# Kernel optimization log

Measured on AMD Instinct MI355X. Metric: run time of the kernel, lower is better.

Reference implementation:

```python
import jax, jax.numpy as jnp
import numpy as np

B, N, D, R, K, H, ORD = 2, 64, 256, 128, 16, 256, 3


def _ln(x, g, b, eps=1e-5):
    m = jnp.mean(x, -1, keepdims=True)
    v = jnp.mean((x - m) ** 2, -1, keepdims=True)
    return (x - m) * jax.lax.rsqrt(v + eps) * g + b


def _legendre(x, order):
    # Legendre polynomials P0..P_order via Bonnet recurrence, stacked on last dim
    p = [jnp.ones_like(x), x]
    for n in range(2, order + 1):
        p.append(((2 * n - 1) * x * p[-1] - (n - 1) * p[-2]) / n)
    return jnp.stack(p[: order + 1], axis=-1)


def _mlp(x, w1, b1, w2, b2):
    return jax.nn.silu(x @ w1 + b1) @ w2 + b2


def setup_inputs() -> dict:
    key = jax.random.key(0)
    ks = iter(jax.random.split(key, 40))

    def nrm(shape, s=0.02):
        return jax.random.normal(next(ks), shape, jnp.float32) * s

    node_s = jax.random.normal(next(ks), (B, N, D), jnp.float32)
    dist = jax.random.uniform(next(ks), (B, N, N), jnp.float32, 0.5, 6.0)
    dist = (dist + jnp.swapaxes(dist, 1, 2)) / 2.0  # symmetric distances
    rbf = jax.random.normal(next(ks), (B, N, N, R), jnp.float32)
    rh = jax.random.normal(next(ks), (B, N, N, 3), jnp.float32)
    r_hat = rh / jnp.clip(jnp.linalg.norm(rh, axis=-1, keepdims=True), 1e-6)
    access_mask = jnp.ones((B, N, N), dtype=bool)
    return dict(
        node_s=node_s, dist=dist, rbf=rbf, r_hat=r_hat, access_mask=access_mask,
        ep_w1=nrm((2 * D + R, H)), ep_b1=jnp.zeros(H), ep_w2=nrm((H, D)), ep_b2=jnp.zeros(D),
        tp_w1=nrm((ORD + 1 + R, H)), tp_b1=jnp.zeros(H), tp_w2=nrm((H, D)), tp_b2=jnp.zeros(D),
        ts_w1=nrm((2 * D, H)), ts_b1=jnp.zeros(H), ts_w2=nrm((H, 1)), ts_b2=jnp.zeros(1),
        mix_ln_g=jnp.ones(2 * D), mix_ln_b=jnp.zeros(2 * D),
        mix_w1=nrm((2 * D, H)), mix_b1=jnp.zeros(H), mix_w2=nrm((H, D)), mix_b2=jnp.zeros(D),
        gate_w=nrm((D, D)), gate_b=jnp.zeros(D),
        node_ln_g=jnp.ones(D), node_ln_b=jnp.zeros(D), node_w=nrm((D, D)), node_b=jnp.zeros(D),
        edge_ln_g=jnp.ones(D), edge_ln_b=jnp.zeros(D),
    )


def reference(node_s, dist, rbf, r_hat, access_mask,
              ep_w1, ep_b1, ep_w2, ep_b2,
              tp_w1, tp_b1, tp_w2, tp_b2,
              ts_w1, ts_b1, ts_w2, ts_b2,
              mix_ln_g, mix_ln_b, mix_w1, mix_b1, mix_w2, mix_b2,
              gate_w, gate_b,
              node_ln_g, node_ln_b, node_w, node_b,
              edge_ln_g, edge_ln_b):
    b, n, d = node_s.shape
    access = access_mask.astype(node_s.dtype)
    # edge base: cat(src, dst, rbf) -> MLP, masked
    src = jnp.broadcast_to(node_s[:, :, None, :], (b, n, n, d))
    dst = jnp.broadcast_to(node_s[:, None, :, :], (b, n, n, d))
    edge_base = _mlp(jnp.concatenate([src, dst, rbf], -1), ep_w1, ep_b1, ep_w2, ep_b2)
    edge_base = edge_base * access[..., None]
    # topk nearest companions under access mask
    max_dist = jnp.clip(jax.lax.stop_gradient(jnp.max(dist, axis=(1, 2), keepdims=True)), 1.0) + 1.0
    masked_dist = jnp.where(access > 0, dist, max_dist)
    k = min(K, n)
    _, topk_idx = jax.lax.top_k(-masked_dist, k)  # (b,n,k) smallest distances
    topk_mask = jnp.take_along_axis(access, topk_idx, axis=2)
    comp_rhat = jnp.take_along_axis(r_hat, topk_idx[..., None], axis=2)   # (b,n,k,3)
    comp_rbf = jnp.take_along_axis(rbf, topk_idx[..., None], axis=2)      # (b,n,k,R)
    comp_feat = node_s[jnp.arange(b)[:, None, None], topk_idx]            # (b,n,k,d)
    # angles between edge i->j and companion i->k
    cos = jnp.clip(jnp.einsum('bijx,bikx->bijk', r_hat, comp_rhat), -1.0 + 1e-6, 1.0 - 1e-6)
    ang = _legendre(cos, ORD)                                             # (b,n,n,k,ORD+1)
    radial = jnp.broadcast_to(comp_rbf[:, :, None], (b, n, n, k, comp_rbf.shape[-1]))
    tw = _mlp(jnp.concatenate([ang, radial], -1), tp_w1, tp_b1, tp_w2, tp_b2)  # (b,n,n,k,d)
    nf = jnp.broadcast_to(comp_feat[:, :, None], (b, n, n, k, d))
    pm = access[..., None] * topk_mask[:, :, None, :]
    anchor = jnp.arange(n)[None, None, :, None]
    pm = jnp.where(anchor == topk_idx[:, :, None, :], 0.0, pm)           # drop k == j
    tpair = tw * nf
    logits = _mlp(jnp.concatenate([tw, nf], -1), ts_w1, ts_b1, ts_w2, ts_b2)[..., 0]
    logits = jnp.where(pm > 0, logits, -jnp.inf)
    attn = jax.nn.softmax(logits, axis=3)
    attn = jnp.where(pm > 0, attn, 0.0)
    t_attn = jnp.einsum('bijkd,bijk->bijd', tpair, attn)
    mpair = jnp.where(pm[..., None] > 0, tpair, -jnp.inf)
    tmax = jnp.max(mpair, axis=3)
    tmax = jnp.where(jnp.isfinite(tmax), tmax, 0.0)
    ctx = _mlp(_ln(jnp.concatenate([t_attn, tmax], -1), mix_ln_g, mix_ln_b), mix_w1, mix_b1, mix_w2, mix_b2)
    ef = _ln(edge_base + ctx, edge_ln_g, edge_ln_b)
    ef = jax.nn.sigmoid(ef @ gate_w + gate_b) * ef
    node_delta = _ln((ef * access[..., None]).sum(2), node_ln_g, node_ln_b) @ node_w + node_b
    denom = jnp.clip(access.sum((1, 2)), 1.0)[:, None]
    bond_graph = ef.sum((1, 2)) / denom
    return node_delta, bond_graph
```

## Files before the change

kernel.cpp:

```cpp
#include <hip/hip_runtime.h>
#include <hip/hip_fp16.h>
#include <math.h>

#define BB 2
#define NN 64
#define DD 256
#define RR 128
#define KK 16
#define HH 256
#define NE (BB*NN*NN)
#define BN (BB*NN)
#define RB 16
#define LROW 264
#define XROW 648
#define YROW 520
#define HROW 264

typedef _Float16 f16;
typedef _Float16 half8 __attribute__((ext_vector_type(8)));
typedef float    f32x4 __attribute__((ext_vector_type(4)));

__device__ __forceinline__ float silu_f(float x){ return x / (1.f + __expf(-x)); }

__device__ __forceinline__ void gemm_tile(const f16* Abase, int astride, const f16* pack,
                                          int KS, int lane, int w, f32x4 acc4[4]){
    int quad = lane >> 4, n = lane & 15;
    for (int ks = 0; ks < KS; ks++){
        half8 a = *(const half8*)(Abase + n*astride + ks*32 + quad*8);
        #pragma unroll
        for (int nti = 0; nti < 4; nti++){
            int ntg = w*4 + nti;
            half8 bfr = *(const half8*)(pack + ((size_t)(ntg*KS + ks)*64 + lane)*8);
            acc4[nti] = __builtin_amdgcn_mfma_f32_16x16x32_f16(a, bfr, acc4[nti], 0, 0, 0);
        }
    }
}

__global__ void k_topk(const float* __restrict__ dist, int* __restrict__ topk_idx){
    int bi = blockIdx.x;
    int lane = threadIdx.x;
    float v = dist[(size_t)bi*NN + lane];
    int idx = lane;
    for (int s = 0; s < KK; s++){
        float bv = v; int bid = idx;
        #pragma unroll
        for (int o = 32; o >= 1; o >>= 1){
            float ov = __shfl_down(bv, o, 64);
            int   oi = __shfl_down(bid, o, 64);
            if (ov < bv || (ov == bv && oi < bid)){ bv = ov; bid = oi; }
        }
        bid = __shfl(bid, 0, 64);
        if (lane == s) topk_idx[bi*KK + s] = bid;
        if (idx == bid) v = INFINITY;
    }
}

__global__ void k_packall(const float* __restrict__ tp_w2, const float* __restrict__ ts_w1,
                          const float* __restrict__ ep_w1, const float* __restrict__ ep_w2,
                          const float* __restrict__ mw1, const float* __restrict__ mw2,
                          const float* __restrict__ gw,
                          f16* packB, f16* packC, f16* packE1, f16* packE2,
                          f16* packM1, f16* packM2, f16* packG){
    int bid = blockIdx.x;
    const float* src; f16* dst; int KS; int fi;
    if      (bid < 128)          { src=tp_w2; dst=packB;  KS=8;  fi=bid; }
    else if ((bid-=128) < 128)   { src=ts_w1; dst=packC;  KS=8;  fi=bid; }
    else if ((bid-=128) < 320)   { src=ep_w1; dst=packE1; KS=20; fi=bid; }
    else if ((bid-=320) < 128)   { src=ep_w2; dst=packE2; KS=8;  fi=bid; }
    else if ((bid-=128) < 256)   { src=mw1;   dst=packM1; KS=16; fi=bid; }
    else if ((bid-=256) < 128)   { src=mw2;   dst=packM2; KS=8;  fi=bid; }
    else                         { src=gw;    dst=packG;  KS=8;  fi=bid-128; }
    int nt = fi / KS, ks = fi % KS;
    int l = threadIdx.x;
    int quad = l >> 4, nn = l & 15;
    size_t base = ((size_t)(nt*KS + ks)*64 + l)*8;
    #pragma unroll
    for (int jj = 0; jj < 8; jj++){
        int k = ks*32 + quad*8 + jj;
        dst[base + jj] = (f16)src[(size_t)k*HH + nt*16 + nn];
    }
}

__global__ void k_precomp(const float* __restrict__ node_s, const float* __restrict__ rbf,
                          const int* __restrict__ topk_idx,
                          const float* __restrict__ tp_w1, const float* __restrict__ ts_w1,
                          f16* __restrict__ rad_h, f16* __restrict__ nf_h){
    int blk = blockIdx.x;
    int bi = blk >> 4; int b = bi >> 6;
    int jk = topk_idx[blk];
    __shared__ __align__(16) float srbf[RR];
    __shared__ __align__(16) float sft[DD];
    int t = threadIdx.x;
    if (t < RR) srbf[t] = rbf[((size_t)bi*NN + jk)*RR + t];
    sft[t] = node_s[(size_t)(b*NN + jk)*DD + t];
    __syncthreads();
    float a1 = 0.f;
    for (int u = 0; u < RR; u++)
        a1 += srbf[u] * tp_w1[(size_t)(4+u)*HH + t];
    rad_h[(size_t)blk*HH + t] = (f16)a1;
    float a2 = 0.f;
    for (int u = 0; u < DD; u++)
        a2 += sft[u] * ts_w1[(size_t)(DD+u)*HH + t];
    nf_h[(size_t)blk*HH + t] = (f16)a2;
}

__global__ __launch_bounds__(256) void k_e1(
        const float* __restrict__ node_s, const float* __restrict__ r_hat,
        const int* __restrict__ topk_idx,
        const f16* __restrict__ rad_h, const f16* __restrict__ nf_h,
        const f16* __restrict__ packB, const f16* __restrict__ packC,
        const float* __restrict__ tp_w1, const float* __restrict__ tp_b1,
        const float* __restrict__ tp_b2,
        const float* __restrict__ ts_b1, const float* __restrict__ ts_w2,
        const float* __restrict__ ts_b2,
        f16* __restrict__ cat){
    int e = blockIdx.x;
    int j = e & (NN-1); int bi = e >> 6; int b = bi >> 6;
    int t = threadIdx.x;
    int lane = t & 63, w = t >> 6;
    int quad = lane >> 4, n = lane & 15;

    __shared__ __align__(16) f16 h1_lds[KK*LROW];
    __shared__ __align__(16) f16 tw_lds[KK*LROW];
    __shared__ __align__(16) f16 nfh_lds[KK*LROW];
    __shared__ float s_ang[KK*4];
    __shared__ float s_pm[KK];
    __shared__ int   s_idx[KK];
    __shared__ float s_logit[KK];
    __shared__ float s_red[4*KK];

    if (t < KK){
        int idxk = topk_idx[bi*KK + t];
        s_idx[t] = idxk;
        s_pm[t] = (idxk == j) ? 0.f : 1.f;
        size_t rj = ((size_t)bi*NN + j)*3, rk = ((size_t)bi*NN + idxk)*3;
        float c = r_hat[rj+0]*r_hat[rk+0] + r_hat[rj+1]*r_hat[rk+1] + r_hat[rj+2]*r_hat[rk+2];
        c = fminf(fmaxf(c, -1.f + 1e-6f), 1.f - 1e-6f);
        float p2 = (3.f*c*c - 1.f)*0.5f;
        float p3 = (5.f*c*p2 - 2.f*c)*(1.f/3.f);
        s_ang[t*4+0] = 1.f; s_ang[t*4+1] = c; s_ang[t*4+2] = p2; s_ang[t*4+3] = p3;
    }
    {
        const f16* nfh = nf_h + (size_t)bi*KK*HH;
        #pragma unroll
        for (int kk = 0; kk < KK; kk++)
            nfh_lds[kk*LROW + t] = nfh[kk*HH + t];
    }
    __syncthreads();

    {
        float b1v = tp_b1[t];
        float w0 = tp_w1[t],        w1v = tp_w1[HH+t];
        float w2v = tp_w1[2*HH+t],  w3v = tp_w1[3*HH+t];
        const f16* rad = rad_h + (size_t)bi*KK*HH;
        #pragma unroll
        for (int kk = 0; kk < KK; kk++){
            float a = b1v + (float)rad[kk*HH + t]
                    + s_ang[kk*4+0]*w0 + s_ang[kk*4+1]*w1v
                    + s_ang[kk*4+2]*w2v + s_ang[kk*4+3]*w3v;
            h1_lds[kk*LROW + t] = (f16)silu_f(a);
        }
    }
    __syncthreads();

    {
        f32x4 acc4[4];
        #pragma unroll
        for (int nti = 0; nti < 4; nti++) acc4[nti] = (f32x4){0.f,0.f,0.f,0.f};
        gemm_tile(h1_lds, LROW, packB, 8, lane, w, acc4);
        #pragma unroll
        for (int nti = 0; nti < 4; nti++){
            int col = w*64 + nti*16 + n;
            float b2v = tp_b2[col];
            #pragma unroll
            for (int reg = 0; reg < 4; reg++)
                tw_lds[(quad*4+reg)*LROW + col] = (f16)(acc4[nti][reg] + b2v);
        }
    }
    __syncthreads();

    float part[4] = {0.f, 0.f, 0.f, 0.f};
    {
        f32x4 acc4[4];
        #pragma unroll
        for (int nti = 0; nti < 4; nti++) acc4[nti] = (f32x4){0.f,0.f,0.f,0.f};
        gemm_tile(tw_lds, LROW, packC, 8, lane, w, acc4);
        #pragma unroll
        for (int nti = 0; nti < 4; nti++){
            int hp = w*64 + nti*16 + n;
            float b1s = ts_b1[hp];
            float w2s = ts_w2[hp];
            #pragma unroll
            for (int reg = 0; reg < 4; reg++){
                int kk = quad*4 + reg;
                float g = acc4[nti][reg] + (float)nfh_lds[kk*LROW + hp] + b1s;
                part[reg] += silu_f(g) * w2s;
            }
        }
    }
    #pragma unroll
    for (int reg = 0; reg < 4; reg++){
        #pragma unroll
        for (int msk = 1; msk < 16; msk <<= 1)
            part[reg] += __shfl_xor(part[reg], msk, 64);
    }
    if (n == 0){
        #pragma unroll
        for (int reg = 0; reg < 4; reg++)
            s_red[w*16 + quad*4 + reg] = part[reg];
    }
    __syncthreads();
    if (t < KK)
        s_logit[t] = s_red[t] + s_red[16+t] + s_red[32+t] + s_red[48+t] + ts_b2[0];
    __syncthreads();

    float attn[KK];
    float m = -INFINITY;
    #pragma unroll
    for (int kk = 0; kk < KK; kk++) if (s_pm[kk] > 0.f) m = fmaxf(m, s_logit[kk]);
    float esum = 0.f;
    #pragma unroll
    for (int kk = 0; kk < KK; kk++){
        float ev = (s_pm[kk] > 0.f) ? __expf(s_logit[kk] - m) : 0.f;
        attn[kk] = ev; esum += ev;
    }
    float inv = (esum > 0.f) ? 1.f/esum : 0.f;
    float ta = 0.f, tmv = -INFINITY;
    #pragma unroll
    for (int kk = 0; kk < KK; kk++){
        float twv = (float)tw_lds[kk*LROW + t];
        float nfv = node_s[(size_t)(b*NN + s_idx[kk])*DD + t];
        float tp = twv * nfv;
        ta += attn[kk] * tp;
        if (s_pm[kk] > 0.f) tmv = fmaxf(tmv, tp);
    }
    ta *= inv;
    if (tmv == -INFINITY) tmv = 0.f;
    cat[(size_t)e*(2*DD) + t]      = (f16)ta;
    cat[(size_t)e*(2*DD) + DD + t] = (f16)tmv;
}

__global__ __launch_bounds__(256) void k_ebmix(
        const float* __restrict__ node_s, const float* __restrict__ rbf,
        const f16* __restrict__ cat,
        const f16* __restrict__ packE1, const f16* __restrict__ packE2,
        const f16* __restrict__ packM1, const f16* __restrict__ packM2,
        const f16* __restrict__ packG,
        const float* __restrict__ ep_b1, const float* __restrict__ ep_b2,
        const float* __restrict__ mg, const float* __restrict__ mbv,
        const float* __restrict__ mb1, const float* __restrict__ mb2,
        const float* __restrict__ gb,
        const float* __restrict__ eg, const float* __restrict__ ebb,
        float* __restrict__ rowsum){
    int blk = blockIdx.x;
    int e0i = blk * RB;
    int bi = e0i >> 6; int b = bi >> 6; int i = bi & (NN-1); int j0 = e0i & (NN-1);
    int t = threadIdx.x;
    int lane = t & 63, w = t >> 6;
    int quad = lane >> 4, n = lane & 15;

    __shared__ __align__(16) f16 BUF1[RB*XROW];
    __shared__ __align__(16) f16 BUF2[RB*HROW];
    __shared__ float s_scr2[RB*8];
    float* BUF1f = (float*)BUF1;

    {
        float vsrc = node_s[(size_t)(b*NN+i)*DD + t];
        #pragma unroll
        for (int r = 0; r < RB; r++){
            BUF1[r*XROW + t]      = (f16)vsrc;
            BUF1[r*XROW + DD + t] = (f16)node_s[(size_t)(b*NN + j0 + r)*DD + t];
        }
        if (t < RR){
            #pragma unroll
            for (int r = 0; r < RB; r++)
                BUF1[r*XROW + 2*DD + t] = (f16)rbf[(size_t)(e0i + r)*RR + t];
        }
    }
    __syncthreads();

    f32x4 acc4[4];
    #pragma unroll
    for (int nti = 0; nti < 4; nti++) acc4[nti] = (f32x4){0.f,0.f,0.f,0.f};
    gemm_tile(BUF1, XROW, packE1, 20, lane, w, acc4);
    #pragma unroll
    for (int nti = 0; nti < 4; nti++){
        int col = w*64 + nti*16 + n;
        float bv = ep_b1[col];
        #pragma unroll
        for (int reg = 0; reg < 4; reg++)
            BUF2[(quad*4+reg)*HROW + col] = (f16)silu_f(acc4[nti][reg] + bv);
    }
    __syncthreads();

    float eb[16];
    #pragma unroll
    for (int nti = 0; nti < 4; nti++) acc4[nti] = (f32x4){0.f,0.f,0.f,0.f};
    gemm_tile(BUF2, HROW, packE2, 8, lane, w, acc4);
    #pragma unroll
    for (int nti = 0; nti < 4; nti++){
        int col = w*64 + nti*16 + n;
        float bv = ep_b2[col];
        #pragma unroll
        for (int reg = 0; reg < 4; reg++)
            eb[nti*4+reg] = acc4[nti][reg] + bv;
    }

    float x0a[RB], x1a[RB];
    {
        #pragma unroll
        for (int r = 0; r < RB; r++){
            size_t base = (size_t)(e0i + r)*(2*DD);
            float x0 = (float)cat[base + t];
            float x1 = (float)cat[base + DD + t];
            x0a[r] = x0; x1a[r] = x1;
            float s = x0 + x1, q2 = x0*x0 + x1*x1;
            #pragma unroll
            for (int o = 32; o >= 1; o >>= 1){ s += __shfl_down(s, o, 64); q2 += __shfl_down(q2, o, 64); }
            if (lane == 0){ s_scr2[r*8 + w*2] = s; s_scr2[r*8 + w*2 + 1] = q2; }
        }
    }
    __syncthreads();
    {
        float g0 = mg[t], g1 = mg[DD+t], b0 = mbv[t], b1 = mbv[DD+t];
        #pragma unroll
        for (int r = 0; r < RB; r++){
            float su = s_scr2[r*8+0]+s_scr2[r*8+2]+s_scr2[r*8+4]+s_scr2[r*8+6];
            float sq = s_scr2[r*8+1]+s_scr2[r*8+3]+s_scr2[r*8+5]+s_scr2[r*8+7];
            float mean = su * (1.f/(2*DD));
            float var  = sq * (1.f/(2*DD)) - mean*mean;
            float rstd = rsqrtf(var + 1e-5f);
            BUF1[r*YROW + t]      = (f16)((x0a[r]-mean)*rstd*g0 + b0);
            BUF1[r*YROW + DD + t] = (f16)((x1a[r]-mean)*rstd*g1 + b1);
        }
    }
    __syncthreads();

    #pragma unroll
    for (int nti = 0; nti < 4; nti++) acc4[nti] = (f32x4){0.f,0.f,0.f,0.f};
    gemm_tile(BUF1, YROW, packM1, 16, lane, w, acc4);
    __syncthreads();
    #pragma unroll
    for (int nti = 0; nti < 4; nti++){
        int col = w*64 + nti*16 + n;
        float bv = mb1[col];
        #pragma unroll
        for (int reg = 0; reg < 4; reg++)
            BUF2[(quad*4+reg)*HROW + col] = (f16)silu_f(acc4[nti][reg] + bv);
    }
    __syncthreads();

    #pragma unroll
    for (int nti = 0; nti < 4; nti++) acc4[nti] = (f32x4){0.f,0.f,0.f,0.f};
    gemm_tile(BUF2, HROW, packM2, 8, lane, w, acc4);
    __syncthreads();
    #pragma unroll
    for (int nti = 0; nti < 4; nti++){
        int col = w*64 + nti*16 + n;
        float bv = mb2[col];
        #pragma unroll
        for (int reg = 0; reg < 4; reg++)
            BUF1f[(quad*4+reg)*264 + col] = acc4[nti][reg] + bv + eb[nti*4+reg];
    }
    __syncthreads();

    {
        #pragma unroll
        for (int r = 0; r < RB; r++){
            float v = BUF1f[r*264 + t];
            float s = v, q2 = v*v;
            #pragma unroll
            for (int o = 32; o >= 1; o >>= 1){ s += __shfl_down(s, o, 64); q2 += __shfl_down(q2, o, 64); }
            if (lane == 0){ s_scr2[r*8 + w*2] = s; s_scr2[r*8 + w*2 + 1] = q2; }
        }
    }
    __syncthreads();
    {
        float gv = eg[t], bv = ebb[t];
        #pragma unroll
        for (int r = 0; r < RB; r++){
            float su = s_scr2[r*8+0]+s_scr2[r*8+2]+s_scr2[r*8+4]+s_scr2[r*8+6];
            float sq = s_scr2[r*8+1]+s_scr2[r*8+3]+s_scr2[r*8+5]+s_scr2[r*8+7];
            float mean = su * (1.f/DD);
            float var  = sq * (1.f/DD) - mean*mean;
            float rstd = rsqrtf(var + 1e-5f);
            BUF2[r*HROW + t] = (f16)((BUF1f[r*264 + t]-mean)*rstd*gv + bv);
        }
    }
    __syncthreads();

    #pragma unroll
    for (int nti = 0; nti < 4; nti++) acc4[nti] = (f32x4){0.f,0.f,0.f,0.f};
    gemm_tile(BUF2, HROW, packG, 8, lane, w, acc4);
    {
        float part[4];
        #pragma unroll
        for (int nti = 0; nti < 4; nti++){
            int col = w*64 + nti*16 + n;
            float gbv = gb[col];
            float s = 0.f;
            #pragma unroll
            for (int reg = 0; reg < 4; reg++){
                int row = quad*4 + reg;
                float gs = 1.f/(1.f + __expf(-(acc4[nti][reg] + gbv)));
                s += gs * (float)BUF2[row*HROW + col];
            }
            part[nti] = s;
        }
        #pragma unroll
        for (int nti = 0; nti < 4; nti++){
            part[nti] += __shfl_xor(part[nti], 16, 64);
            part[nti] += __shfl_xor(part[nti], 32, 64);
        }
        if (quad == 0){
            #pragma unroll
            for (int nti = 0; nti < 4; nti++)
                atomicAdd(&rowsum[(size_t)bi*DD + w*64 + nti*16 + n], part[nti]);
        }
    }
}

__global__ void k_node(const float* __restrict__ rowsum, const float* __restrict__ g,
                       const float* __restrict__ bvec, const float* __restrict__ nw,
                       const float* __restrict__ nb, float* __restrict__ out){
    int bi = blockIdx.x; int t = threadIdx.x;
    __shared__ __align__(16) float s_y[DD];
    __shared__ float scr[8];
    float s = rowsum[(size_t)bi*DD + t];
    float a = s, q = s*s;
    #pragma unroll
    for (int o = 32; o >= 1; o >>= 1){ a += __shfl_down(a, o, 64); q += __shfl_down(q, o, 64); }
    if ((t&63) == 0){ scr[(t>>6)*2] = a; scr[(t>>6)*2+1] = q; }
    __syncthreads();
    float su = scr[0]+scr[2]+scr[4]+scr[6];
    float sq = scr[1]+scr[3]+scr[5]+scr[7];
    float mean = su * (1.f/DD);
    float var  = sq * (1.f/DD) - mean*mean;
    float rstd = rsqrtf(var + 1e-5f);
    s_y[t] = (s-mean)*rstd*g[t] + bvec[t];
    __syncthreads();
    float o = nb[t];
    for (int u = 0; u < DD; u++)
        o += s_y[u]*nw[(size_t)u*DD + t];
    out[(size_t)bi*DD + t] = o;
}

__global__ void k_bond(const float* __restrict__ rowsum, float* __restrict__ out){
    int b = blockIdx.x; int t = threadIdx.x;
    float s = 0.f;
    for (int i = 0; i < NN; i++) s += rowsum[(size_t)(b*NN+i)*DD + t];
    out[(size_t)BB*NN*DD + b*DD + t] = s * (1.f/4096.f);
}

extern "C" void kernel_launch(void* const* d_in, const int* in_sizes, int n_in,
                              void* d_out, int out_size, void* d_ws, size_t ws_size,
                              hipStream_t stream){
    const float* node_s = (const float*)d_in[0];
    const float* dist   = (const float*)d_in[1];
    const float* rbf    = (const float*)d_in[2];
    const float* r_hat  = (const float*)d_in[3];
    const float* ep_w1 = (const float*)d_in[5];
    const float* ep_b1 = (const float*)d_in[6];
    const float* ep_w2 = (const float*)d_in[7];
    const float* ep_b2 = (const float*)d_in[8];
    const float* tp_w1 = (const float*)d_in[9];
    const float* tp_b1 = (const float*)d_in[10];
    const float* tp_w2 = (const float*)d_in[11];
    const float* tp_b2 = (const float*)d_in[12];
    const float* ts_w1 = (const float*)d_in[13];
    const float* ts_b1 = (const float*)d_in[14];
    const float* ts_w2 = (const float*)d_in[15];
    const float* ts_b2 = (const float*)d_in[16];
    const float* mix_ln_g = (const float*)d_in[17];
    const float* mix_ln_b = (const float*)d_in[18];
    const float* mix_w1 = (const float*)d_in[19];
    const float* mix_b1 = (const float*)d_in[20];
    const float* mix_w2 = (const float*)d_in[21];
    const float* mix_b2 = (const float*)d_in[22];
    const float* gate_w = (const float*)d_in[23];
    const float* gate_b = (const float*)d_in[24];
    const float* node_ln_g = (const float*)d_in[25];
    const float* node_ln_b = (const float*)d_in[26];
    const float* node_w = (const float*)d_in[27];
    const float* node_b = (const float*)d_in[28];
    const float* edge_ln_g = (const float*)d_in[29];
    const float* edge_ln_b = (const float*)d_in[30];

    char* wsb = (char*)d_ws;
    int*   topk_idx = (int*)wsb;
    f16*   rad_h    = (f16*)(wsb + 8192);
    f16*   nf_h     = (f16*)(wsb + 8192 + (1u<<20));
    f16*   cat      = (f16*)(wsb + 8192 + (2u<<20));
    float* rowsum   = (float*)(wsb + 8192 + (10u<<20));
    size_t off = 8192 + (10u<<20) + 131072;
    f16* packB  = (f16*)(wsb + off); off += 131072;
    f16* packC  = (f16*)(wsb + off); off += 131072;
    f16* packE1 = (f16*)(wsb + off); off += 327680;
    f16* packE2 = (f16*)(wsb + off); off += 131072;
    f16* packM1 = (f16*)(wsb + off); off += 262144;
    f16* packM2 = (f16*)(wsb + off); off += 131072;
    f16* packG  = (f16*)(wsb + off); off += 131072;

    float* out = (float*)d_out;

    hipMemsetAsync(rowsum, 0, (size_t)BN*DD*sizeof(float), stream);
    hipLaunchKernelGGL(k_topk,    dim3(BN),    dim3(64),  0, stream, dist, topk_idx);
    hipLaunchKernelGGL(k_packall, dim3(1216),  dim3(64),  0, stream,
                       tp_w2, ts_w1, ep_w1, ep_w2, mix_w1, mix_w2, gate_w,
                       packB, packC, packE1, packE2, packM1, packM2, packG);
    hipLaunchKernelGGL(k_precomp, dim3(BN*KK), dim3(256), 0, stream, node_s, rbf, topk_idx, tp_w1, ts_w1, rad_h, nf_h);
    hipLaunchKernelGGL(k_e1,      dim3(NE),    dim3(256), 0, stream,
                       node_s, r_hat, topk_idx, rad_h, nf_h, packB, packC,
                       tp_w1, tp_b1, tp_b2, ts_b1, ts_w2, ts_b2, cat);
    hipLaunchKernelGGL(k_ebmix,   dim3(NE/RB), dim3(256), 0, stream,
                       node_s, rbf, cat, packE1, packE2, packM1, packM2, packG,
                       ep_b1, ep_b2, mix_ln_g, mix_ln_b, mix_b1, mix_b2,
                       gate_b, edge_ln_g, edge_ln_b, rowsum);
    hipLaunchKernelGGL(k_node, dim3(BN), dim3(256), 0, stream, rowsum, node_ln_g, node_ln_b, node_w, node_b, out);
    hipLaunchKernelGGL(k_bond, dim3(BB), dim3(256), 0, stream, rowsum, out);
}
```

Baseline: 320.4 us.

## Batch multiple edges per block in k_e1 and multiple k rows in k_precomp

```diff
diff --git a/kernel.cpp b/kernel.cpp
--- a/kernel.cpp
+++ b/kernel.cpp
@@ -11,6 +11,7 @@
 #define NE (BB*NN*NN)
 #define BN (BB*NN)
 #define RB 16
+#define EB 16
 #define LROW 264
 #define XROW 648
 #define YROW 520
@@ -86,22 +87,34 @@
                           const float* __restrict__ tp_w1, const float* __restrict__ ts_w1,
                           f16* __restrict__ rad_h, f16* __restrict__ nf_h){
     int blk = blockIdx.x;
-    int bi = blk >> 4; int b = bi >> 6;
-    int jk = topk_idx[blk];
-    __shared__ __align__(16) float srbf[RR];
-    __shared__ __align__(16) float sft[DD];
+    int bi = blk >> 1; int ko = (blk & 1)*8; int b = bi >> 6;
     int t = threadIdx.x;
-    if (t < RR) srbf[t] = rbf[((size_t)bi*NN + jk)*RR + t];
-    sft[t] = node_s[(size_t)(b*NN + jk)*DD + t];
-    __syncthreads();
-    float a1 = 0.f;
-    for (int u = 0; u < RR; u++)
-        a1 += srbf[u] * tp_w1[(size_t)(4+u)*HH + t];
-    rad_h[(size_t)blk*HH + t] = (f16)a1;
-    float a2 = 0.f;
-    for (int u = 0; u < DD; u++)
-        a2 += sft[u] * ts_w1[(size_t)(DD+u)*HH + t];
-    nf_h[(size_t)blk*HH + t] = (f16)a2;
+    __shared__ __align__(16) float srbf[8][RR];
+    __shared__ __align__(16) float sft[8][DD];
+    for (int kk = 0; kk < 8; kk++){
+        int jk = topk_idx[bi*KK + ko + kk];
+        if (t < RR) srbf[kk][t] = rbf[((size_t)bi*NN + jk)*RR + t];
+        sft[kk][t] = node_s[(size_t)(b*NN + jk)*DD + t];
+    }
+    __syncthreads();
+    float a1[8] = {0,0,0,0,0,0,0,0};
+    for (int u = 0; u < RR; u++){
+        float w = tp_w1[(size_t)(4+u)*HH + t];
+        #pragma unroll
+        for (int kk = 0; kk < 8; kk++) a1[kk] += srbf[kk][u] * w;
+    }
+    #pragma unroll
+    for (int kk = 0; kk < 8; kk++)
+        rad_h[(size_t)(bi*KK + ko + kk)*HH + t] = (f16)a1[kk];
+    float a2[8] = {0,0,0,0,0,0,0,0};
+    for (int u = 0; u < DD; u++){
+        float w = ts_w1[(size_t)(DD+u)*HH + t];
+        #pragma unroll
+        for (int kk = 0; kk < 8; kk++) a2[kk] += sft[kk][u] * w;
+    }
+    #pragma unroll
+    for (int kk = 0; kk < 8; kk++)
+        nf_h[(size_t)(bi*KK + ko + kk)*HH + t] = (f16)a2[kk];
 }
 
 __global__ __launch_bounds__(256) void k_e1(
@@ -109,135 +122,194 @@
         const int* __restrict__ topk_idx,
         const f16* __restrict__ rad_h, const f16* __restrict__ nf_h,
         const f16* __restrict__ packB, const f16* __restrict__ packC,
-        const float* __restrict__ tp_w1, const float* __restrict__ tp_b1,
+        const float* __restrict__ tp_b1, const float* __restrict__ tp_w1,
         const float* __restrict__ tp_b2,
         const float* __restrict__ ts_b1, const float* __restrict__ ts_w2,
         const float* __restrict__ ts_b2,
         f16* __restrict__ cat){
-    int e = blockIdx.x;
-    int j = e & (NN-1); int bi = e >> 6; int b = bi >> 6;
+    int blk = blockIdx.x;
+    int bi = blk >> 2; int j0 = (blk & 3)*EB; int b = bi >> 6;
     int t = threadIdx.x;
     int lane = t & 63, w = t >> 6;
     int quad = lane >> 4, n = lane & 15;
 
-    __shared__ __align__(16) f16 h1_lds[KK*LROW];
-    __shared__ __align__(16) f16 tw_lds[KK*LROW];
+    __shared__ __align__(16) f16 rad_lds[KK*LROW];
     __shared__ __align__(16) f16 nfh_lds[KK*LROW];
-    __shared__ float s_ang[KK*4];
-    __shared__ float s_pm[KK];
+    __shared__ __align__(16) f16 nf_lds[KK*LROW];
+    __shared__ __align__(16) f16 h1_lds[2*KK*LROW];
+    __shared__ __align__(16) f16 tw_lds[2*KK*LROW];
+    __shared__ __align__(16) float4 P_lds[EB*KK];
+    __shared__ float s_pmall[EB*KK];
     __shared__ int   s_idx[KK];
-    __shared__ float s_logit[KK];
-    __shared__ float s_red[4*KK];
-
-    if (t < KK){
-        int idxk = topk_idx[bi*KK + t];
-        s_idx[t] = idxk;
-        s_pm[t] = (idxk == j) ? 0.f : 1.f;
+    __shared__ float s_logit[2*KK];
+    __shared__ float s_red[2*64];
+
+    if (t < KK) s_idx[t] = topk_idx[bi*KK + t];
+    __syncthreads();
+
+    {
+        const f16* rad = rad_h + (size_t)bi*KK*HH;
+        const f16* nfh = nf_h + (size_t)bi*KK*HH;
+        #pragma unroll
+        for (int k = 0; k < KK; k++){
+            rad_lds[k*LROW + t] = rad[k*HH + t];
+            nfh_lds[k*LROW + t] = nfh[k*HH + t];
+            nf_lds[k*LROW + t]  = (f16)node_s[(size_t)(b*NN + s_idx[k])*DD + t];
+        }
+    }
+    {
+        int ej = t >> 4, k = t & 15;
+        int j = j0 + ej;
+        int idxk = s_idx[k];
         size_t rj = ((size_t)bi*NN + j)*3, rk = ((size_t)bi*NN + idxk)*3;
         float c = r_hat[rj+0]*r_hat[rk+0] + r_hat[rj+1]*r_hat[rk+1] + r_hat[rj+2]*r_hat[rk+2];
         c = fminf(fmaxf(c, -1.f + 1e-6f), 1.f - 1e-6f);
         float p2 = (3.f*c*c - 1.f)*0.5f;
         float p3 = (5.f*c*p2 - 2.f*c)*(1.f/3.f);
-        s_ang[t*4+0] = 1.f; s_ang[t*4+1] = c; s_ang[t*4+2] = p2; s_ang[t*4+3] = p3;
-    }
-    {
-        const f16* nfh = nf_h + (size_t)bi*KK*HH;
-        #pragma unroll
-        for (int kk = 0; kk < KK; kk++)
-            nfh_lds[kk*LROW + t] = nfh[kk*HH + t];
-    }
-    __syncthreads();
-
-    {
-        float b1v = tp_b1[t];
-        float w0 = tp_w1[t],        w1v = tp_w1[HH+t];
-        float w2v = tp_w1[2*HH+t],  w3v = tp_w1[3*HH+t];
-        const f16* rad = rad_h + (size_t)bi*KK*HH;
-        #pragma unroll
-        for (int kk = 0; kk < KK; kk++){
-            float a = b1v + (float)rad[kk*HH + t]
-                    + s_ang[kk*4+0]*w0 + s_ang[kk*4+1]*w1v
-                    + s_ang[kk*4+2]*w2v + s_ang[kk*4+3]*w3v;
-            h1_lds[kk*LROW + t] = (f16)silu_f(a);
-        }
-    }
-    __syncthreads();
-
-    {
-        f32x4 acc4[4];
-        #pragma unroll
-        for (int nti = 0; nti < 4; nti++) acc4[nti] = (f32x4){0.f,0.f,0.f,0.f};
-        gemm_tile(h1_lds, LROW, packB, 8, lane, w, acc4);
-        #pragma unroll
-        for (int nti = 0; nti < 4; nti++){
-            int col = w*64 + nti*16 + n;
-            float b2v = tp_b2[col];
-            #pragma unroll
-            for (int reg = 0; reg < 4; reg++)
-                tw_lds[(quad*4+reg)*LROW + col] = (f16)(acc4[nti][reg] + b2v);
-        }
-    }
-    __syncthreads();
-
-    float part[4] = {0.f, 0.f, 0.f, 0.f};
-    {
-        f32x4 acc4[4];
-        #pragma unroll
-        for (int nti = 0; nti < 4; nti++) acc4[nti] = (f32x4){0.f,0.f,0.f,0.f};
-        gemm_tile(tw_lds, LROW, packC, 8, lane, w, acc4);
-        #pragma unroll
-        for (int nti = 0; nti < 4; nti++){
-            int hp = w*64 + nti*16 + n;
-            float b1s = ts_b1[hp];
-            float w2s = ts_w2[hp];
-            #pragma unroll
-            for (int reg = 0; reg < 4; reg++){
-                int kk = quad*4 + reg;
-                float g = acc4[nti][reg] + (float)nfh_lds[kk*LROW + hp] + b1s;
-                part[reg] += silu_f(g) * w2s;
-            }
-        }
-    }
-    #pragma unroll
-    for (int reg = 0; reg < 4; reg++){
-        #pragma unroll
-        for (int msk = 1; msk < 16; msk <<= 1)
-            part[reg] += __shfl_xor(part[reg], msk, 64);
-    }
-    if (n == 0){
-        #pragma unroll
-        for (int reg = 0; reg < 4; reg++)
-            s_red[w*16 + quad*4 + reg] = part[reg];
-    }
-    __syncthreads();
-    if (t < KK)
-        s_logit[t] = s_red[t] + s_red[16+t] + s_red[32+t] + s_red[48+t] + ts_b2[0];
-    __syncthreads();
-
-    float attn[KK];
-    float m = -INFINITY;
-    #pragma unroll
-    for (int kk = 0; kk < KK; kk++) if (s_pm[kk] > 0.f) m = fmaxf(m, s_logit[kk]);
-    float esum = 0.f;
-    #pragma unroll
-    for (int kk = 0; kk < KK; kk++){
-        float ev = (s_pm[kk] > 0.f) ? __expf(s_logit[kk] - m) : 0.f;
-        attn[kk] = ev; esum += ev;
-    }
-    float inv = (esum > 0.f) ? 1.f/esum : 0.f;
-    float ta = 0.f, tmv = -INFINITY;
-    #pragma unroll
-    for (int kk = 0; kk < KK; kk++){
-        float twv = (float)tw_lds[kk*LROW + t];
-        float nfv = node_s[(size_t)(b*NN + s_idx[kk])*DD + t];
-        float tp = twv * nfv;
-        ta += attn[kk] * tp;
-        if (s_pm[kk] > 0.f) tmv = fmaxf(tmv, tp);
-    }
-    ta *= inv;
-    if (tmv == -INFINITY) tmv = 0.f;
-    cat[(size_t)e*(2*DD) + t]      = (f16)ta;
-    cat[(size_t)e*(2*DD) + DD + t] = (f16)tmv;
+        P_lds[ej*KK + k] = make_float4(1.f, c, p2, p3);
+        s_pmall[ej*KK + k] = (idxk == j) ? 0.f : 1.f;
+    }
+    __syncthreads();
+
+    float b1v = tp_b1[t];
+    float w0 = tp_w1[t], w1v = tp_w1[HH+t], w2v = tp_w1[2*HH+t], w3v = tp_w1[3*HH+t];
+    float b2c[4], b1c[4], w2c[4];
+    #pragma unroll
+    for (int nti = 0; nti < 4; nti++){
+        int col = w*64 + nti*16 + n;
+        b2c[nti] = tp_b2[col];
+        b1c[nti] = ts_b1[col];
+        w2c[nti] = ts_w2[col];
+    }
+    float tb2 = ts_b2[0];
+
+    for (int g = 0; g < EB/2; g++){
+        #pragma unroll
+        for (int e = 0; e < 2; e++){
+            int ej = 2*g + e;
+            #pragma unroll
+            for (int k = 0; k < KK; k++){
+                float4 P = P_lds[ej*KK + k];
+                float a = b1v + (float)rad_lds[k*LROW + t]
+                        + P.x*w0 + P.y*w1v + P.z*w2v + P.w*w3v;
+                h1_lds[e*KK*LROW + k*LROW + t] = (f16)silu_f(a);
+            }
+        }
+        __syncthreads();
+
+        {
+            f32x4 acc[2][4];
+            #pragma unroll
+            for (int e = 0; e < 2; e++)
+                #pragma unroll
+                for (int nti = 0; nti < 4; nti++) acc[e][nti] = (f32x4){0.f,0.f,0.f,0.f};
+            for (int ks = 0; ks < 8; ks++){
+                half8 a0 = *(const half8*)(h1_lds + n*LROW + ks*32 + quad*8);
+                half8 a1 = *(const half8*)(h1_lds + KK*LROW + n*LROW + ks*32 + quad*8);
+                #pragma unroll
+                for (int nti = 0; nti < 4; nti++){
+                    half8 bfr = *(const half8*)(packB + ((size_t)((w*4+nti)*8 + ks)*64 + lane)*8);
+                    acc[0][nti] = __builtin_amdgcn_mfma_f32_16x16x32_f16(a0, bfr, acc[0][nti], 0, 0, 0);
+                    acc[1][nti] = __builtin_amdgcn_mfma_f32_16x16x32_f16(a1, bfr, acc[1][nti], 0, 0, 0);
+                }
+            }
+            #pragma unroll
+            for (int e = 0; e < 2; e++)
+                #pragma unroll
+                for (int nti = 0; nti < 4; nti++){
+                    int col = w*64 + nti*16 + n;
+                    #pragma unroll
+                    for (int reg = 0; reg < 4; reg++)
+                        tw_lds[e*KK*LROW + (quad*4+reg)*LROW + col] = (f16)(acc[e][nti][reg] + b2c[nti]);
+                }
+        }
+        __syncthreads();
+
+        {
+            f32x4 acc[2][4];
+            #pragma unroll
+            for (int e = 0; e < 2; e++)
+                #pragma unroll
+                for (int nti = 0; nti < 4; nti++) acc[e][nti] = (f32x4){0.f,0.f,0.f,0.f};
+            for (int ks = 0; ks < 8; ks++){
+                half8 a0 = *(const half8*)(tw_lds + n*LROW + ks*32 + quad*8);
+                half8 a1 = *(const half8*)(tw_lds + KK*LROW + n*LROW + ks*32 + quad*8);
+                #pragma unroll
+                for (int nti = 0; nti < 4; nti++){
+                    half8 bfr = *(const half8*)(packC + ((size_t)((w*4+nti)*8 + ks)*64 + lane)*8);
+                    acc[0][nti] = __builtin_amdgcn_mfma_f32_16x16x32_f16(a0, bfr, acc[0][nti], 0, 0, 0);
+                    acc[1][nti] = __builtin_amdgcn_mfma_f32_16x16x32_f16(a1, bfr, acc[1][nti], 0, 0, 0);
+                }
+            }
+            float part[2][4] = {{0,0,0,0},{0,0,0,0}};
+            #pragma unroll
+            for (int e = 0; e < 2; e++)
+                #pragma unroll
+                for (int nti = 0; nti < 4; nti++){
+                    int col = w*64 + nti*16 + n;
+                    #pragma unroll
+                    for (int reg = 0; reg < 4; reg++){
+                        int k = quad*4 + reg;
+                        float gv = acc[e][nti][reg] + (float)nfh_lds[k*LROW + col] + b1c[nti];
+                        part[e][reg] += silu_f(gv) * w2c[nti];
+                    }
+                }
+            #pragma unroll
+            for (int e = 0; e < 2; e++)
+                #pragma unroll
+                for (int reg = 0; reg < 4; reg++){
+                    #pragma unroll
+                    for (int msk = 1; msk < 16; msk <<= 1)
+                        part[e][reg] += __shfl_xor(part[e][reg], msk, 64);
+                }
+            if (n == 0){
+                #pragma unroll
+                for (int e = 0; e < 2; e++)
+                    #pragma unroll
+                    for (int reg = 0; reg < 4; reg++)
+                        s_red[e*64 + w*16 + quad*4 + reg] = part[e][reg];
+            }
+        }
+        __syncthreads();
+        if (t < 2*KK){
+            int e = t >> 4, k = t & 15;
+            s_logit[e*KK + k] = s_red[e*64 + k] + s_red[e*64 + 16 + k]
+                              + s_red[e*64 + 32 + k] + s_red[e*64 + 48 + k] + tb2;
+        }
+        __syncthreads();
+
+        #pragma unroll
+        for (int e = 0; e < 2; e++){
+            int ej = 2*g + e;
+            const float* pm = s_pmall + ej*KK;
+            const float* lg = s_logit + e*KK;
+            float m = -INFINITY;
+            #pragma unroll
+            for (int k = 0; k < KK; k++) if (pm[k] > 0.f) m = fmaxf(m, lg[k]);
+            float attn[KK]; float esum = 0.f;
+            #pragma unroll
+            for (int k = 0; k < KK; k++){
+                float ev = (pm[k] > 0.f) ? __expf(lg[k] - m) : 0.f;
+                attn[k] = ev; esum += ev;
+            }
+            float inv = (esum > 0.f) ? 1.f/esum : 0.f;
+            float ta = 0.f, tmv = -INFINITY;
+            #pragma unroll
+            for (int k = 0; k < KK; k++){
+                float twv = (float)tw_lds[e*KK*LROW + k*LROW + t];
+                float nfv = (float)nf_lds[k*LROW + t];
+                float tp = twv * nfv;
+                ta += attn[k] * tp;
+                if (pm[k] > 0.f) tmv = fmaxf(tmv, tp);
+            }
+            ta *= inv;
+            if (tmv == -INFINITY) tmv = 0.f;
+            size_t ge = (size_t)(bi*NN + j0 + ej);
+            cat[ge*(2*DD) + t]      = (f16)ta;
+            cat[ge*(2*DD) + DD + t] = (f16)tmv;
+        }
+        __syncthreads();
+    }
 }
 
 __global__ __launch_bounds__(256) void k_ebmix(
@@ -508,10 +580,10 @@
     hipLaunchKernelGGL(k_packall, dim3(1216),  dim3(64),  0, stream,
                        tp_w2, ts_w1, ep_w1, ep_w2, mix_w1, mix_w2, gate_w,
                        packB, packC, packE1, packE2, packM1, packM2, packG);
-    hipLaunchKernelGGL(k_precomp, dim3(BN*KK), dim3(256), 0, stream, node_s, rbf, topk_idx, tp_w1, ts_w1, rad_h, nf_h);
-    hipLaunchKernelGGL(k_e1,      dim3(NE),    dim3(256), 0, stream,
+    hipLaunchKernelGGL(k_precomp, dim3(BN*2),  dim3(256), 0, stream, node_s, rbf, topk_idx, tp_w1, ts_w1, rad_h, nf_h);
+    hipLaunchKernelGGL(k_e1,      dim3(NE/EB), dim3(256), 0, stream,
                        node_s, r_hat, topk_idx, rad_h, nf_h, packB, packC,
-                       tp_w1, tp_b1, tp_b2, ts_b1, ts_w2, ts_b2, cat);
+                       tp_b1, tp_w1, tp_b2, ts_b1, ts_w2, ts_b2, cat);
     hipLaunchKernelGGL(k_ebmix,   dim3(NE/RB), dim3(256), 0, stream,
                        node_s, rbf, cat, packE1, packE2, packM1, packM2, packG,
                        ep_b1, ep_b2, mix_ln_g, mix_ln_b, mix_b1, mix_b2,
```

After: 374.4 us. +16.8%, slower.
